# Performance work log

Measured on AMD Instinct MI355X. Metric: run time of the kernel, lower is better.

Reference implementation:

```python
import jax, jax.numpy as jnp
import numpy as np

B, C, H, W = 4, 256, 64, 64
CK = C // 8   # 32, theta/phi channels
CV = C // 2   # 128, g channels


def setup_inputs() -> dict:
    key = jax.random.key(0)
    ks = jax.random.split(key, 10)
    s = lambda fan: 1.0 / np.sqrt(fan)
    inp = {
        "x": jax.random.normal(ks[0], (B, C, H, W), dtype=jnp.float32),
        "theta_w": jax.random.normal(ks[1], (CK, C), dtype=jnp.float32) * s(C),
        "theta_b": jax.random.normal(ks[2], (CK,), dtype=jnp.float32) * 0.01,
        "phi_w": jax.random.normal(ks[3], (CK, C), dtype=jnp.float32) * s(C),
        "phi_b": jax.random.normal(ks[4], (CK,), dtype=jnp.float32) * 0.01,
        "g_w": jax.random.normal(ks[5], (CV, C), dtype=jnp.float32) * s(C),
        "g_b": jax.random.normal(ks[6], (CV,), dtype=jnp.float32) * 0.01,
        "o_w": jax.random.normal(ks[7], (C, CV), dtype=jnp.float32) * s(CV),
        "o_b": jax.random.normal(ks[8], (C,), dtype=jnp.float32) * 0.01,
        "gamma": jax.random.normal(ks[9], (1,), dtype=jnp.float32) * 0.1,
    }
    return inp


def reference(x, theta_w, theta_b, phi_w, phi_b, g_w, g_b, o_w, o_b, gamma):
    b, c, h, w = x.shape
    n = h * w
    xf = x.reshape(b, c, n)  # [B, C, N]
    # 1x1 convs == per-pixel linear projections
    theta = jnp.einsum('oc,bcn->bon', theta_w, xf) + theta_b[None, :, None]  # [B, CK, N]
    phi = jnp.einsum('oc,bcn->bon', phi_w, xf) + phi_b[None, :, None]        # [B, CK, N]
    g = jnp.einsum('oc,bcn->bon', g_w, xf) + g_b[None, :, None]              # [B, CV, N]
    # scores[b, i, j] = theta_i . phi_j ; softmax over dim=1 (query axis i) as in torch code
    scores = jnp.einsum('bci,bcj->bij', theta, phi)  # [B, N, N]
    attention = jax.nn.softmax(scores, axis=1)
    # o_pre = bmm(g, attention^T): o_pre[b, c, i] = sum_j g[b, c, j] * attention[b, i, j]
    o_pre = jnp.einsum('bcj,bij->bci', g, attention)  # [B, CV, N]
    o = jnp.einsum('oc,bcn->bon', o_w, o_pre) + o_b[None, :, None]  # [B, C, N]
    out = (gamma[0] * o + xf).reshape(b, c, h, w)
    return out
```

## Files before the change

### kernel.cpp

```cpp
#include <hip/hip_runtime.h>
#include <math.h>

#define B_  4
#define C_  256
#define N_  4096
#define CK_ 32
#define CV_ 128

typedef __attribute__((ext_vector_type(8))) short short8;
typedef __attribute__((ext_vector_type(4))) float f32x4;
typedef unsigned short u16;
typedef unsigned int   u32;

static constexpr float LOG2E = 1.4426950408889634f;

static __device__ __forceinline__ u16 f2bf(float f) {
    u32 u = __float_as_uint(f);
    u = (u + 0x7FFFu + ((u >> 16) & 1u)) >> 16;
    return (u16)u;
}
static __device__ __forceinline__ float bf2f(u16 h) {
    return __uint_as_float(((u32)h) << 16);
}

__global__ __launch_bounds__(256) void wconv_kernel(
    const float* __restrict__ theta_w, const float* __restrict__ phi_w,
    const float* __restrict__ g_w,     const float* __restrict__ o_w,
    u16* __restrict__ W16, u16* __restrict__ ow16)
{
    const int idx = blockIdx.x * 256 + threadIdx.x;
    if (idx < 8192)        W16[idx] = f2bf(theta_w[idx] * LOG2E);
    else if (idx < 16384)  W16[idx] = f2bf(phi_w[idx - 8192]);
    else if (idx < 49152)  W16[idx] = f2bf(g_w[idx - 16384]);
    else                   ow16[idx - 49152] = f2bf(o_w[idx - 49152]);
}

__global__ __launch_bounds__(256) void xt_kernel(
    const float* __restrict__ x, u16* __restrict__ xT16)
{
    const int b = blockIdx.z, c0 = blockIdx.y * 64, n0 = blockIdx.x * 64;
    const int t = threadIdx.x;
    __shared__ float tile[64][65];

    const int cr = t >> 4, nc = (t & 15) * 4;
    #pragma unroll
    for (int it = 0; it < 4; ++it) {
        const float4 v = *(const float4*)(x + (size_t)(b * C_ + c0 + cr + it * 16) * N_ + n0 + nc);
        tile[cr + it * 16][nc + 0] = v.x; tile[cr + it * 16][nc + 1] = v.y;
        tile[cr + it * 16][nc + 2] = v.z; tile[cr + it * 16][nc + 3] = v.w;
    }
    __syncthreads();
    const int n = t >> 2, cg = (t & 3) * 16;
    union { u16 us[16]; uint4 u4[2]; } pk;
    #pragma unroll
    for (int e = 0; e < 16; ++e) pk.us[e] = f2bf(tile[cg + e][n]);
    uint4* dst = (uint4*)(xT16 + (size_t)(b * N_ + n0 + n) * C_ + c0 + cg);
    dst[0] = pk.u4[0]; dst[1] = pk.u4[1];
}

__global__ __launch_bounds__(256) void proj_mfma_kernel(
    const u16* __restrict__ xT16, const u16* __restrict__ W16,
    const float* __restrict__ theta_b, const float* __restrict__ phi_b,
    const float* __restrict__ g_b,
    u16* __restrict__ theta_t, u16* __restrict__ phi_t, u16* __restrict__ g16)
{
    const int b = blockIdx.y, n0 = blockIdx.x * 64;
    const int w = threadIdx.x >> 6, lane = threadIdx.x & 63;
    const int lr = lane & 15, q = lane >> 4;
    const f32x4 zf = {0.f, 0.f, 0.f, 0.f};

    const u16* xrow = xT16 + (size_t)(b * N_ + n0 + w * 16 + lr) * C_;
    f32x4 acc[4];
    #pragma unroll
    for (int nt = 0; nt < 4; ++nt) acc[nt] = zf;
    for (int ks = 0; ks < 8; ++ks) {
        const short8 aX = *(const short8*)(xrow + ks * 32 + q * 8);
        #pragma unroll
        for (int nt = 0; nt < 4; ++nt) {
            const short8 bW = *(const short8*)(W16 + (size_t)(nt * 16 + lr) * C_ + ks * 32 + q * 8);
            acc[nt] = __builtin_amdgcn_mfma_f32_16x16x32_bf16(aX, bW, acc[nt], 0, 0, 0);
        }
    }
    #pragma unroll
    for (int nt = 0; nt < 4; ++nt) {
        const int o = nt * 16 + lr;
        #pragma unroll
        for (int reg = 0; reg < 4; ++reg) {
            const int n = n0 + w * 16 + q * 4 + reg;
            if (nt < 2)
                theta_t[(size_t)(b * N_ + n) * CK_ + o] = f2bf(acc[nt][reg] + theta_b[o] * LOG2E);
            else
                phi_t[(size_t)(b * N_ + n) * CK_ + (o - 32)] = f2bf(acc[nt][reg] + phi_b[o - 32]);
        }
    }

    #pragma unroll
    for (int mp = 0; mp < 2; ++mp) {
        const int crow = (w * 2 + mp) * 16;
        f32x4 ag[4];
        #pragma unroll
        for (int nt = 0; nt < 4; ++nt) ag[nt] = zf;
        for (int ks = 0; ks < 8; ++ks) {
            const short8 aW = *(const short8*)(W16 + (size_t)(64 + crow + lr) * C_ + ks * 32 + q * 8);
            #pragma unroll
            for (int nt = 0; nt < 4; ++nt) {
                const short8 bX = *(const short8*)(xT16 + (size_t)(b * N_ + n0 + nt * 16 + lr) * C_ + ks * 32 + q * 8);
                ag[nt] = __builtin_amdgcn_mfma_f32_16x16x32_bf16(aW, bX, ag[nt], 0, 0, 0);
            }
        }
        #pragma unroll
        for (int nt = 0; nt < 4; ++nt) {
            #pragma unroll
            for (int reg = 0; reg < 4; ++reg) {
                const int c = crow + q * 4 + reg;
                const int n = n0 + nt * 16 + lr;
                g16[(size_t)(b * CV_ + c) * N_ + n] = f2bf(ag[nt][reg] + g_b[c]);
            }
        }
    }
}

__global__ __launch_bounds__(256) void colstats_kernel(
    const u16* __restrict__ theta_t, const u16* __restrict__ phi_t,
    float* __restrict__ Z)
{
    const int b  = blockIdx.z;
    const int j0 = blockIdx.x * 32;
    const int istart = blockIdx.y * (N_ / 4);
    const int tid = threadIdx.x;
    const int wave = tid >> 6, lane = tid & 63;
    const int lr = lane & 15, q = lane >> 4;

    const int jW = j0 + (wave & 1) * 16;
    const short8 bF = *(const short8*)(phi_t + (size_t)(b * N_ + jW + lr) * CK_ + q * 8);

    const u16* thp = theta_t + (size_t)b * N_ * CK_;
    const f32x4 zero = {0.f, 0.f, 0.f, 0.f};
    float zacc = 0.f;
    for (int it = istart + (wave >> 1) * 16; it < istart + N_ / 4; it += 32) {
        const short8 aF = *(const short8*)(thp + (size_t)(it + lr) * CK_ + q * 8);
        f32x4 S = __builtin_amdgcn_mfma_f32_16x16x32_bf16(aF, bF, zero, 0, 0, 0);
        zacc += exp2f(S[0]) + exp2f(S[1]) + exp2f(S[2]) + exp2f(S[3]);
    }
    zacc += __shfl_xor(zacc, 16);
    zacc += __shfl_xor(zacc, 32);
    if (lane < 16) atomicAdd(&Z[(size_t)b * N_ + jW + lr], zacc);
}

__global__ __launch_bounds__(256) void gscale_kernel(
    u16* __restrict__ g16, const float* __restrict__ Z)
{
    const size_t idx = ((size_t)blockIdx.x * 256 + threadIdx.x) * 8;
    const int n = (int)(idx & (N_ - 1));
    const int b = (int)(idx / ((size_t)CV_ * N_));
    uint4 raw = *(const uint4*)(g16 + idx);
    const float4 z0 = *(const float4*)(Z + (size_t)b * N_ + n);
    const float4 z1 = *(const float4*)(Z + (size_t)b * N_ + n + 4);
    const float zz[8] = {z0.x, z0.y, z0.z, z0.w, z1.x, z1.y, z1.z, z1.w};
    u16* pr = (u16*)&raw;
    union { u16 us[8]; uint4 u4; } pk;
    #pragma unroll
    for (int k = 0; k < 8; ++k) pk.us[k] = f2bf(bf2f(pr[k]) / zz[k]);
    *(uint4*)(g16 + idx) = pk.u4;
}

__global__ __launch_bounds__(512, 4) void opre_kernel(
    const u16* __restrict__ theta_t, const u16* __restrict__ phi_t,
    const u16* __restrict__ g16, float* __restrict__ o_p0, float* __restrict__ o_p1)
{
    const int b = blockIdx.z, jh = blockIdx.y, i0 = blockIdx.x * 64;
    const int w = threadIdx.x >> 6, lane = threadIdx.x & 63;
    const int lr = lane & 15, q = lane >> 4;

    __shared__ u16 El[2][64 * 64];
    __shared__ float rp[16 * 132];

    const int jt = w & 3, it2 = w >> 2;
    const short8 aF0 = *(const short8*)(theta_t + (size_t)(b * N_ + i0 + it2 * 32 + lr) * CK_ + q * 8);
    const short8 aF1 = *(const short8*)(theta_t + (size_t)(b * N_ + i0 + it2 * 32 + 16 + lr) * CK_ + q * 8);

    const int cw = w * 16;
    const u16* gb = g16 + (size_t)(b * CV_ + cw + lr) * N_;
    const u16* pb = phi_t + (size_t)(b * N_) * CK_;

    const f32x4 zf = {0.f, 0.f, 0.f, 0.f};
    f32x4 acc[4];
    #pragma unroll
    for (int nt = 0; nt < 4; ++nt) acc[nt] = zf;

    const int jstart = jh * (N_ / 2), jend = jstart + N_ / 2;
    short8 bF = *(const short8*)(pb + (size_t)(jstart + jt * 16 + lr) * CK_ + q * 8);
    int buf = 0;

    for (int j0 = jstart; j0 < jend; j0 += 64) {
        const short8 gA0 = *(const short8*)(gb + j0 + q * 8);
        const short8 gA1 = *(const short8*)(gb + j0 + 32 + q * 8);

        const f32x4 S0 = __builtin_amdgcn_mfma_f32_16x16x32_bf16(aF0, bF, zf, 0, 0, 0);
        const f32x4 S1 = __builtin_amdgcn_mfma_f32_16x16x32_bf16(aF1, bF, zf, 0, 0, 0);

        const int jn = (j0 + 64 < jend) ? j0 + 64 : jstart;
        bF = *(const short8*)(pb + (size_t)(jn + jt * 16 + lr) * CK_ + q * 8);

        u16* Eb = El[buf];
        const int jcol = jt * 16 + lr;
        #pragma unroll
        for (int reg = 0; reg < 4; ++reg) {
            const int ia = it2 * 32 + q * 4 + reg;
            Eb[ia * 64 + ((((jcol >> 3) ^ (ia & 7)) << 3) | (jcol & 7))] = f2bf(exp2f(S0[reg]));
            const int ib = ia + 16;
            Eb[ib * 64 + ((((jcol >> 3) ^ (ib & 7)) << 3) | (jcol & 7))] = f2bf(exp2f(S1[reg]));
        }
        __syncthreads();

        #pragma unroll
        for (int nt = 0; nt < 4; ++nt) {
            const int row = nt * 16 + lr;
            const short8 bE0 = *(const short8*)(Eb + row * 64 + ((q ^ (row & 7)) << 3));
            const short8 bE1 = *(const short8*)(Eb + row * 64 + (((4 + q) ^ (row & 7)) << 3));
            acc[nt] = __builtin_amdgcn_mfma_f32_16x16x32_bf16(gA0, bE0, acc[nt], 0, 0, 0);
            acc[nt] = __builtin_amdgcn_mfma_f32_16x16x32_bf16(gA1, bE1, acc[nt], 0, 0, 0);
        }
        buf ^= 1;
    }

    __syncthreads();
    float* op = (jh ? o_p1 : o_p0) + (size_t)(b * N_ + i0) * CV_;
    #pragma unroll
    for (int p = 0; p < 4; ++p) {
        #pragma unroll
        for (int reg = 0; reg < 4; ++reg)
            rp[lr * 132 + cw + q * 4 + reg] = acc[p][reg];
        __syncthreads();
        const int t = threadIdx.x;
        const int ir = t >> 5, cc = (t & 31) * 4;
        *(float4*)(op + (size_t)(p * 16 + ir) * CV_ + cc) = *(const float4*)(rp + ir * 132 + cc);
        __syncthreads();
    }
}

__global__ __launch_bounds__(256) void final_mfma_kernel(
    const float* __restrict__ o_p0, const float* __restrict__ o_p1,
    const u16* __restrict__ ow16, const float* __restrict__ o_b,
    const float* __restrict__ gamma, const float* __restrict__ x,
    float* __restrict__ out)
{
    const int b = blockIdx.y, n0 = blockIdx.x * 64;
    const int w = threadIdx.x >> 6, lane = threadIdx.x & 63;
    const int lr = lane & 15, q = lane >> 4;
    const f32x4 zf = {0.f, 0.f, 0.f, 0.f};

    f32x4 acc[4][4];
    #pragma unroll
    for (int mt = 0; mt < 4; ++mt)
        #pragma unroll
        for (int nt = 0; nt < 4; ++nt) acc[mt][nt] = zf;

    const float* p0 = o_p0 + (size_t)(b * N_ + n0) * CV_;
    const float* p1 = o_p1 + (size_t)(b * N_ + n0) * CV_;

    for (int ks = 0; ks < 4; ++ks) {
        short8 bP[4];
        #pragma unroll
        for (int nt = 0; nt < 4; ++nt) {
            const size_t base = (size_t)(nt * 16 + lr) * CV_ + ks * 32 + q * 8;
            const float4 a0 = *(const float4*)(p0 + base);
            const float4 a1 = *(const float4*)(p0 + base + 4);
            const float4 b0 = *(const float4*)(p1 + base);
            const float4 b1 = *(const float4*)(p1 + base + 4);
            union { u16 us[8]; short8 s8; } pk;
            pk.us[0] = f2bf(a0.x + b0.x); pk.us[1] = f2bf(a0.y + b0.y);
            pk.us[2] = f2bf(a0.z + b0.z); pk.us[3] = f2bf(a0.w + b0.w);
            pk.us[4] = f2bf(a1.x + b1.x); pk.us[5] = f2bf(a1.y + b1.y);
            pk.us[6] = f2bf(a1.z + b1.z); pk.us[7] = f2bf(a1.w + b1.w);
            bP[nt] = pk.s8;
        }
        #pragma unroll
        for (int mt = 0; mt < 4; ++mt) {
            const short8 aW = *(const short8*)(ow16 + (size_t)((w * 4 + mt) * 16 + lr) * CV_ + ks * 32 + q * 8);
            #pragma unroll
            for (int nt = 0; nt < 4; ++nt)
                acc[mt][nt] = __builtin_amdgcn_mfma_f32_16x16x32_bf16(aW, bP[nt], acc[mt][nt], 0, 0, 0);
        }
    }

    const float gm = gamma[0];
    #pragma unroll
    for (int mt = 0; mt < 4; ++mt) {
        #pragma unroll
        for (int nt = 0; nt < 4; ++nt) {
            #pragma unroll
            for (int reg = 0; reg < 4; ++reg) {
                const int oc = (w * 4 + mt) * 16 + q * 4 + reg;
                const int n = n0 + nt * 16 + lr;
                const size_t off = (size_t)(b * C_ + oc) * N_ + n;
                out[off] = x[off] + gm * (acc[mt][nt][reg] + o_b[oc]);
            }
        }
    }
}

extern "C" void kernel_launch(void* const* d_in, const int* in_sizes, int n_in,
                              void* d_out, int out_size, void* d_ws, size_t ws_size,
                              hipStream_t stream)
{
    const float* x       = (const float*)d_in[0];
    const float* theta_w = (const float*)d_in[1];
    const float* theta_b = (const float*)d_in[2];
    const float* phi_w   = (const float*)d_in[3];
    const float* phi_b   = (const float*)d_in[4];
    const float* g_w     = (const float*)d_in[5];
    const float* g_b     = (const float*)d_in[6];
    const float* o_w     = (const float*)d_in[7];
    const float* o_b     = (const float*)d_in[8];
    const float* gamma   = (const float*)d_in[9];
    float* out = (float*)d_out;

    u16* xT16    = (u16*)d_ws;
    u16* W16     = xT16 + (size_t)B_ * N_ * C_;
    u16* ow16    = W16 + 192 * C_;
    u16* theta_t = ow16 + C_ * CV_;
    u16* phi_t   = theta_t + (size_t)B_ * N_ * CK_;
    u16* g16     = phi_t + (size_t)B_ * N_ * CK_;
    float* Z     = (float*)(g16 + (size_t)B_ * CV_ * N_);
    float* o_p0  = Z + (size_t)B_ * N_;
    float* o_p1  = o_p0 + (size_t)B_ * N_ * CV_;

    hipMemsetAsync(Z, 0, (size_t)B_ * N_ * sizeof(float), stream);

    wconv_kernel<<<dim3(320), 256, 0, stream>>>(theta_w, phi_w, g_w, o_w, W16, ow16);
    xt_kernel<<<dim3(N_ / 64, C_ / 64, B_), 256, 0, stream>>>(x, xT16);
    proj_mfma_kernel<<<dim3(N_ / 64, B_), 256, 0, stream>>>(
        xT16, W16, theta_b, phi_b, g_b, theta_t, phi_t, g16);
    colstats_kernel<<<dim3(N_ / 32, 4, B_), 256, 0, stream>>>(theta_t, phi_t, Z);
    gscale_kernel<<<dim3((B_ * CV_ * N_) / 2048), 256, 0, stream>>>(g16, Z);
    opre_kernel<<<dim3(N_ / 64, 2, B_), 512, 0, stream>>>(theta_t, phi_t, g16, o_p0, o_p1);
    final_mfma_kernel<<<dim3(N_ / 64, B_), 256, 0, stream>>>(
        o_p0, o_p1, ow16, o_b, gamma, x, out);
}
```

Measured before the change: 205.4 us.

## Retile opre MFMA work, use fast exp2/rcp intrinsics and packed bf16 conversion

Replaces libm exp2f and the division with the hardware v_exp_f32 and v_rcp_f32 instructions, and uses v_cvt_pk_bf16_f32 for packed bf16 stores. The opre kernel swaps MFMA operand roles so each wave writes its E tile as packed 64-bit stores and computes a 2x2 tile (32 channels x 32 rows) that reuses each E fragment across two g fragments. The LDS swizzle changes to match. The final kernel halves its per-block pixel tile to launch more blocks. The approximate exp and reciprocal slightly change precision.

```diff
diff --git a/kernel.cpp b/kernel.cpp
--- a/kernel.cpp
+++ b/kernel.cpp
@@ -21,6 +21,25 @@
 }
 static __device__ __forceinline__ float bf2f(u16 h) {
     return __uint_as_float(((u32)h) << 16);
+}
+
+static __device__ __forceinline__ float fexp2(float x) {
+#if __has_builtin(__builtin_amdgcn_exp2f)
+    return __builtin_amdgcn_exp2f(x);
+#else
+    float r; asm("v_exp_f32 %0, %1\n\ts_nop 0" : "=v"(r) : "v"(x)); return r;
+#endif
+}
+static __device__ __forceinline__ float frcp(float x) {
+#if __has_builtin(__builtin_amdgcn_rcpf)
+    return __builtin_amdgcn_rcpf(x);
+#else
+    float r; asm("v_rcp_f32 %0, %1\n\ts_nop 0" : "=v"(r) : "v"(x)); return r;
+#endif
+}
+static __device__ __forceinline__ u32 cvt_pk_bf16(float a, float b) {
+    u32 r; asm("v_cvt_pk_bf16_f32 %0, %1, %2" : "=v"(r) : "v"(a), "v"(b));
+    return r;
 }
 
 __global__ __launch_bounds__(256) void wconv_kernel(
@@ -140,7 +159,7 @@
     for (int it = istart + (wave >> 1) * 16; it < istart + N_ / 4; it += 32) {
         const short8 aF = *(const short8*)(thp + (size_t)(it + lr) * CK_ + q * 8);
         f32x4 S = __builtin_amdgcn_mfma_f32_16x16x32_bf16(aF, bF, zero, 0, 0, 0);
-        zacc += exp2f(S[0]) + exp2f(S[1]) + exp2f(S[2]) + exp2f(S[3]);
+        zacc += fexp2(S[0]) + fexp2(S[1]) + fexp2(S[2]) + fexp2(S[3]);
     }
     zacc += __shfl_xor(zacc, 16);
     zacc += __shfl_xor(zacc, 32);
@@ -160,7 +179,7 @@
     u16* pr = (u16*)&raw;
     union { u16 us[8]; uint4 u4; } pk;
     #pragma unroll
-    for (int k = 0; k < 8; ++k) pk.us[k] = f2bf(bf2f(pr[k]) / zz[k]);
+    for (int k = 0; k < 8; ++k) pk.us[k] = f2bf(bf2f(pr[k]) * frcp(zz[k]));
     *(uint4*)(g16 + idx) = pk.u4;
 }
 
@@ -175,51 +194,63 @@
     __shared__ u16 El[2][64 * 64];
     __shared__ float rp[16 * 132];
 
-    const int jt = w & 3, it2 = w >> 2;
-    const short8 aF0 = *(const short8*)(theta_t + (size_t)(b * N_ + i0 + it2 * 32 + lr) * CK_ + q * 8);
-    const short8 aF1 = *(const short8*)(theta_t + (size_t)(b * N_ + i0 + it2 * 32 + 16 + lr) * CK_ + q * 8);
-
-    const int cw = w * 16;
-    const u16* gb = g16 + (size_t)(b * CV_ + cw + lr) * N_;
-    const u16* pb = phi_t + (size_t)(b * N_) * CK_;
+    const int jt = w & 3, ih = w >> 2;
+    const short8 bT0 = *(const short8*)(theta_t + (size_t)(b * N_ + i0 + ih * 32 + lr) * CK_ + q * 8);
+    const short8 bT1 = *(const short8*)(theta_t + (size_t)(b * N_ + i0 + ih * 32 + 16 + lr) * CK_ + q * 8);
+
+    const int cg = w & 3, ig = w >> 2;
+    const u16* gb0 = g16 + (size_t)(b * CV_ + cg * 32 + lr) * N_;
+    const u16* gb1 = gb0 + (size_t)16 * N_;
+    const u16* pb  = phi_t + (size_t)(b * N_) * CK_;
 
     const f32x4 zf = {0.f, 0.f, 0.f, 0.f};
-    f32x4 acc[4];
-    #pragma unroll
-    for (int nt = 0; nt < 4; ++nt) acc[nt] = zf;
+    f32x4 acc[2][2];
+    #pragma unroll
+    for (int mt = 0; mt < 2; ++mt)
+        #pragma unroll
+        for (int nt = 0; nt < 2; ++nt) acc[mt][nt] = zf;
 
     const int jstart = jh * (N_ / 2), jend = jstart + N_ / 2;
-    short8 bF = *(const short8*)(pb + (size_t)(jstart + jt * 16 + lr) * CK_ + q * 8);
+    short8 aP = *(const short8*)(pb + (size_t)(jstart + jt * 16 + lr) * CK_ + q * 8);
     int buf = 0;
 
+    const int sw  = lr & 14;
+    const int wo0 = (ih * 32 + lr) * 64 + (((jt * 4 + q) ^ sw) << 2);
+    const int wo1 = wo0 + 16 * 64;
+    const int ro_row = (ig * 32 + lr) * 64;
+    const int ro_s0  = (((q * 2) + 0) ^ sw) << 2;
+    const int ro_s1  = (((q * 2) + 8) ^ sw) << 2;
+
     for (int j0 = jstart; j0 < jend; j0 += 64) {
-        const short8 gA0 = *(const short8*)(gb + j0 + q * 8);
-        const short8 gA1 = *(const short8*)(gb + j0 + 32 + q * 8);
-
-        const f32x4 S0 = __builtin_amdgcn_mfma_f32_16x16x32_bf16(aF0, bF, zf, 0, 0, 0);
-        const f32x4 S1 = __builtin_amdgcn_mfma_f32_16x16x32_bf16(aF1, bF, zf, 0, 0, 0);
+        const short8 gA00 = *(const short8*)(gb0 + j0 + q * 8);
+        const short8 gA01 = *(const short8*)(gb0 + j0 + 32 + q * 8);
+        const short8 gA10 = *(const short8*)(gb1 + j0 + q * 8);
+        const short8 gA11 = *(const short8*)(gb1 + j0 + 32 + q * 8);
+
+        const f32x4 S0 = __builtin_amdgcn_mfma_f32_16x16x32_bf16(aP, bT0, zf, 0, 0, 0);
+        const f32x4 S1 = __builtin_amdgcn_mfma_f32_16x16x32_bf16(aP, bT1, zf, 0, 0, 0);
 
         const int jn = (j0 + 64 < jend) ? j0 + 64 : jstart;
-        bF = *(const short8*)(pb + (size_t)(jn + jt * 16 + lr) * CK_ + q * 8);
+        aP = *(const short8*)(pb + (size_t)(jn + jt * 16 + lr) * CK_ + q * 8);
 
         u16* Eb = El[buf];
-        const int jcol = jt * 16 + lr;
-        #pragma unroll
-        for (int reg = 0; reg < 4; ++reg) {
-            const int ia = it2 * 32 + q * 4 + reg;
-            Eb[ia * 64 + ((((jcol >> 3) ^ (ia & 7)) << 3) | (jcol & 7))] = f2bf(exp2f(S0[reg]));
-            const int ib = ia + 16;
-            Eb[ib * 64 + ((((jcol >> 3) ^ (ib & 7)) << 3) | (jcol & 7))] = f2bf(exp2f(S1[reg]));
-        }
+        uint2 v0, v1;
+        v0.x = cvt_pk_bf16(fexp2(S0[0]), fexp2(S0[1]));
+        v0.y = cvt_pk_bf16(fexp2(S0[2]), fexp2(S0[3]));
+        v1.x = cvt_pk_bf16(fexp2(S1[0]), fexp2(S1[1]));
+        v1.y = cvt_pk_bf16(fexp2(S1[2]), fexp2(S1[3]));
+        *(uint2*)(Eb + wo0) = v0;
+        *(uint2*)(Eb + wo1) = v1;
         __syncthreads();
 
         #pragma unroll
-        for (int nt = 0; nt < 4; ++nt) {
-            const int row = nt * 16 + lr;
-            const short8 bE0 = *(const short8*)(Eb + row * 64 + ((q ^ (row & 7)) << 3));
-            const short8 bE1 = *(const short8*)(Eb + row * 64 + (((4 + q) ^ (row & 7)) << 3));
-            acc[nt] = __builtin_amdgcn_mfma_f32_16x16x32_bf16(gA0, bE0, acc[nt], 0, 0, 0);
-            acc[nt] = __builtin_amdgcn_mfma_f32_16x16x32_bf16(gA1, bE1, acc[nt], 0, 0, 0);
+        for (int nt = 0; nt < 2; ++nt) {
+            const short8 bE0 = *(const short8*)(Eb + ro_row + nt * (16 * 64) + ro_s0);
+            const short8 bE1 = *(const short8*)(Eb + ro_row + nt * (16 * 64) + ro_s1);
+            acc[0][nt] = __builtin_amdgcn_mfma_f32_16x16x32_bf16(gA00, bE0, acc[0][nt], 0, 0, 0);
+            acc[0][nt] = __builtin_amdgcn_mfma_f32_16x16x32_bf16(gA01, bE1, acc[0][nt], 0, 0, 0);
+            acc[1][nt] = __builtin_amdgcn_mfma_f32_16x16x32_bf16(gA10, bE0, acc[1][nt], 0, 0, 0);
+            acc[1][nt] = __builtin_amdgcn_mfma_f32_16x16x32_bf16(gA11, bE1, acc[1][nt], 0, 0, 0);
         }
         buf ^= 1;
     }
@@ -228,9 +259,14 @@
     float* op = (jh ? o_p1 : o_p0) + (size_t)(b * N_ + i0) * CV_;
     #pragma unroll
     for (int p = 0; p < 4; ++p) {
-        #pragma unroll
-        for (int reg = 0; reg < 4; ++reg)
-            rp[lr * 132 + cw + q * 4 + reg] = acc[p][reg];
+        if (ig == (p >> 1)) {
+            const int nt = p & 1;
+            #pragma unroll
+            for (int mt = 0; mt < 2; ++mt)
+                #pragma unroll
+                for (int reg = 0; reg < 4; ++reg)
+                    rp[lr * 132 + cg * 32 + mt * 16 + q * 4 + reg] = acc[mt][nt][reg];
+        }
         __syncthreads();
         const int t = threadIdx.x;
         const int ir = t >> 5, cc = (t & 31) * 4;
@@ -245,41 +281,41 @@
     const float* __restrict__ gamma, const float* __restrict__ x,
     float* __restrict__ out)
 {
-    const int b = blockIdx.y, n0 = blockIdx.x * 64;
+    const int b = blockIdx.y, n0 = blockIdx.x * 32;
     const int w = threadIdx.x >> 6, lane = threadIdx.x & 63;
     const int lr = lane & 15, q = lane >> 4;
     const f32x4 zf = {0.f, 0.f, 0.f, 0.f};
 
-    f32x4 acc[4][4];
+    f32x4 acc[4][2];
     #pragma unroll
     for (int mt = 0; mt < 4; ++mt)
         #pragma unroll
-        for (int nt = 0; nt < 4; ++nt) acc[mt][nt] = zf;
+        for (int nt = 0; nt < 2; ++nt) acc[mt][nt] = zf;
 
     const float* p0 = o_p0 + (size_t)(b * N_ + n0) * CV_;
     const float* p1 = o_p1 + (size_t)(b * N_ + n0) * CV_;
 
     for (int ks = 0; ks < 4; ++ks) {
-        short8 bP[4];
-        #pragma unroll
-        for (int nt = 0; nt < 4; ++nt) {
+        short8 bP[2];
+        #pragma unroll
+        for (int nt = 0; nt < 2; ++nt) {
             const size_t base = (size_t)(nt * 16 + lr) * CV_ + ks * 32 + q * 8;
             const float4 a0 = *(const float4*)(p0 + base);
             const float4 a1 = *(const float4*)(p0 + base + 4);
-            const float4 b0 = *(const float4*)(p1 + base);
-            const float4 b1 = *(const float4*)(p1 + base + 4);
-            union { u16 us[8]; short8 s8; } pk;
-            pk.us[0] = f2bf(a0.x + b0.x); pk.us[1] = f2bf(a0.y + b0.y);
-            pk.us[2] = f2bf(a0.z + b0.z); pk.us[3] = f2bf(a0.w + b0.w);
-            pk.us[4] = f2bf(a1.x + b1.x); pk.us[5] = f2bf(a1.y + b1.y);
-            pk.us[6] = f2bf(a1.z + b1.z); pk.us[7] = f2bf(a1.w + b1.w);
+            const float4 c0 = *(const float4*)(p1 + base);
+            const float4 c1 = *(const float4*)(p1 + base + 4);
+            union { u32 u[4]; short8 s8; } pk;
+            pk.u[0] = cvt_pk_bf16(a0.x + c0.x, a0.y + c0.y);
+            pk.u[1] = cvt_pk_bf16(a0.z + c0.z, a0.w + c0.w);
+            pk.u[2] = cvt_pk_bf16(a1.x + c1.x, a1.y + c1.y);
+            pk.u[3] = cvt_pk_bf16(a1.z + c1.z, a1.w + c1.w);
             bP[nt] = pk.s8;
         }
         #pragma unroll
         for (int mt = 0; mt < 4; ++mt) {
             const short8 aW = *(const short8*)(ow16 + (size_t)((w * 4 + mt) * 16 + lr) * CV_ + ks * 32 + q * 8);
             #pragma unroll
-            for (int nt = 0; nt < 4; ++nt)
+            for (int nt = 0; nt < 2; ++nt)
                 acc[mt][nt] = __builtin_amdgcn_mfma_f32_16x16x32_bf16(aW, bP[nt], acc[mt][nt], 0, 0, 0);
         }
     }
@@ -288,7 +324,7 @@
     #pragma unroll
     for (int mt = 0; mt < 4; ++mt) {
         #pragma unroll
-        for (int nt = 0; nt < 4; ++nt) {
+        for (int nt = 0; nt < 2; ++nt) {
             #pragma unroll
             for (int reg = 0; reg < 4; ++reg) {
                 const int oc = (w * 4 + mt) * 16 + q * 4 + reg;
@@ -335,6 +371,6 @@
     colstats_kernel<<<dim3(N_ / 32, 4, B_), 256, 0, stream>>>(theta_t, phi_t, Z);
     gscale_kernel<<<dim3((B_ * CV_ * N_) / 2048), 256, 0, stream>>>(g16, Z);
     opre_kernel<<<dim3(N_ / 64, 2, B_), 512, 0, stream>>>(theta_t, phi_t, g16, o_p0, o_p1);
-    final_mfma_kernel<<<dim3(N_ / 64, B_), 256, 0, stream>>>(
+    final_mfma_kernel<<<dim3(N_ / 32, B_), 256, 0, stream>>>(
         o_p0, o_p1, ow16, o_b, gamma, x, out);
 }
```

After: 216.1 us. +5.2%, slower.
